# Performance work log

Measured on AMD Instinct MI355X. Metric: run time of the kernel, lower is better.

Reference implementation:

```python
import jax, jax.numpy as jnp
import numpy as np
from jax import lax

# Config mirrors TemporalLePEAttention(dim=256, resolution=(56,56), idx=0, split_size=4, num_heads=8, temporal=True)
B, T, H, W, C = 2, 2, 56, 56, 256
NH = 8
HD = C // NH
SS = 4                      # split_size
H_sp, W_sp = H, SS          # idx == 0 -> strip windows of full height
nWh, nWw = H // H_sp, W // W_sp   # 1, 14
SCALE = HD ** -0.5
KH, KW = W_sp, H_sp         # unfold kernel = focal_window = [W_sp, H_sp] = (4, 56)
PH, PW = 0, H_sp // 2       # idx == 0 padding = [0, H_sp//2]
NW = B * nWh * nWw          # number of windows
TQ = T * H_sp * W_sp        # query tokens per window


def setup_inputs() -> dict:
    key = jax.random.key(0)
    k1, k2 = jax.random.split(key, 2)
    qkv = jax.random.normal(k1, (3, B, T, H, W, C), jnp.float32)
    # depthwise 3x3 LePE conv (nn.Conv2d(dim, dim, 3, padding=1, groups=dim))
    get_v_w = jax.random.normal(k2, (C, 1, 3, 3), jnp.float32) * 0.1
    get_v_b = jnp.zeros((C,), jnp.float32)
    # pool linear initialized as in the module: weight = SS/(H_sp*W_sp), bias = 0
    pool_w = jnp.full((SS, H_sp * W_sp), SS / (H_sp * W_sp), jnp.float32)
    pool_b = jnp.zeros((SS,), jnp.float32)
    return {"qkv": qkv, "get_v_w": get_v_w, "get_v_b": get_v_b,
            "pool_w": pool_w, "pool_b": pool_b}


def _windows_thw(x):
    # im2ddca_temporal: (B,T,H,W,C) -> (B*nWh*nWw, NH, T*H_sp*W_sp, HD)
    x = x.reshape(B, T, nWh, H_sp, nWw, W_sp, C).transpose(0, 2, 4, 1, 3, 5, 6)
    x = x.reshape(NW, TQ, NH, HD).transpose(0, 2, 1, 3)
    return x


def _lepe_temporal(v, w, b):
    # get_lepe_temporal: window v, depthwise 3x3 conv, return (v_win, lepe) as (NW, NH, TQ, HD)
    xw = v.reshape(B, T, nWh, H_sp, nWw, W_sp, C).transpose(0, 2, 4, 1, 6, 3, 5)
    xw = xw.reshape(-1, C, H_sp, W_sp)  # (B*nWh*nWw*T, C, H_sp, W_sp)
    lepe = lax.conv_general_dilated(xw, w, (1, 1), 'SAME', feature_group_count=C,
                                    dimension_numbers=('NCHW', 'OIHW', 'NCHW'))
    lepe = lepe + b[None, :, None, None]

    def fmt(t):
        t = t.reshape(NW, T, NH, HD, H_sp * W_sp).transpose(0, 2, 1, 4, 3)
        return t.reshape(NW, NH, TQ, HD)
    return fmt(xw), fmt(lepe)


def _pool_unfold(t, pool_w, pool_b):
    # focal pooling: per-window linear over H_sp*W_sp -> SS, then unfold over pooled map
    tw = t.reshape(B, T, nWh, H_sp, nWw, W_sp, C).transpose(0, 2, 4, 1, 6, 3, 5)
    tw = tw.reshape(B, nWh, nWw, T, C, H_sp * W_sp)
    p = jnp.einsum('bhwtcn,sn->bhwtcs', tw, pool_w) + pool_b  # (B,nWh,nWw,T,C,SS)
    # flatten(-2) + permute + reshape -> pooled map (B*T, C, SS*nWh, nWw)  (idx == 0)
    pm = p.transpose(0, 3, 4, 5, 1, 2).reshape(B * T, C, SS * nWh, nWw)
    # nn.Unfold(kernel=(KH,KW), padding=(PH,PW), stride=1); here out_h == 1
    pmp = jnp.pad(pm, ((0, 0), (0, 0), (PH, PH), (PW, PW)))
    ow = pmp.shape[3] - KW + 1  # = nWw + 1
    patches = jnp.stack([pmp[:, :, :, i:i + KW] for i in range(ow)], axis=1)  # (BT, ow, C, KH, KW)
    u = patches.reshape(B, T, ow, C, KH, KW).transpose(0, 2, 1, 4, 5, 3)      # (B, ow, T, KH, KW, C)
    u = u.reshape(B * ow, T * KH * KW, NH, HD).transpose(0, 2, 1, 3)          # (B*ow, NH, Tkk, HD)
    # idx == 0: view (B, nWh, -1, ...) and drop the last unfold location -> one per window
    u = u.reshape(B, nWh, ow // nWh, NH, T * KH * KW, HD)[:, :, :-1]
    return u.reshape(NW, NH, T * KH * KW, HD)


def reference(qkv, get_v_w, get_v_b, pool_w, pool_b):
    q_in, k_in, v_in = qkv[0], qkv[1], qkv[2]
    q = _windows_thw(q_in) * SCALE                      # (NW, NH, TQ, HD)
    k = _windows_thw(k_in)
    v, lepe = _lepe_temporal(v_in, get_v_w, get_v_b)
    kp = _pool_unfold(k_in, pool_w, pool_b)             # (NW, NH, TQ, HD)
    vp = _pool_unfold(v_in, pool_w, pool_b)
    k = jnp.concatenate([k, kp], axis=2)                # (NW, NH, 2*TQ, HD)
    v = jnp.concatenate([v, vp], axis=2)
    attn = jax.nn.softmax(jnp.einsum('wnqd,wnkd->wnqk', q, k), axis=-1)
    x = jnp.einsum('wnqk,wnkd->wnqd', attn, v) + lepe   # (NW, NH, TQ, HD)
    x = x.transpose(0, 2, 1, 3).reshape(NW, TQ, C)
    # windows2img_temporal -> (B, T, H, W, C)
    x = x.reshape(B, nWh, nWw, T, H_sp, W_sp, C).transpose(0, 3, 1, 4, 2, 5, 6)
    return x.reshape(B, T, H, W, C)
```

## Files before the change

kernel.cpp:

```cpp
#include <hip/hip_runtime.h>
#include <hip/hip_bf16.h>

#define B_    2
#define T_    2
#define H_    56
#define W_    56
#define C_    256
#define NWW_  14
#define WC_   (W_ * C_)
#define P1_   (H_ * W_ * C_)
#define NWIN_ 448
#define NPOOL_ 128
#define VIRT_ 320.0f
#define MEXP_ 16.0f

typedef __bf16 bf16;
typedef __bf16 bf16x8 __attribute__((ext_vector_type(8)));
typedef __bf16 bf16x4 __attribute__((ext_vector_type(4)));
typedef float  f32x4  __attribute__((ext_vector_type(4)));
typedef short  s16x4  __attribute__((ext_vector_type(4)));
typedef short  s16x8  __attribute__((ext_vector_type(8)));
typedef unsigned int  uint;
typedef uint   uint4v __attribute__((ext_vector_type(4)));
typedef uint   uint2v __attribute__((ext_vector_type(2)));
typedef unsigned short u16;

__device__ __forceinline__ uint pack2(float a, float b) {
    u16 ha = __builtin_bit_cast(u16, (bf16)a);
    u16 hb = __builtin_bit_cast(u16, (bf16)b);
    return (uint)ha | ((uint)hb << 16);
}
__device__ __forceinline__ s16x4 pack4(float a, float b, float c, float d) {
    const uint2v u = {pack2(a, b), pack2(c, d)};
    return __builtin_bit_cast(s16x4, u);
}

__launch_bounds__(1024, 1)
__global__ void pre_kernel(const float* __restrict__ k_in, const float* __restrict__ v_in,
                           const float* __restrict__ pool_w, const float* __restrict__ pool_b,
                           const float* __restrict__ gw, const float* __restrict__ gb,
                           bf16* __restrict__ kw, bf16* __restrict__ vw,
                           bf16* __restrict__ lepew, bf16* __restrict__ kp,
                           bf16* __restrict__ vp) {
    __shared__ float pws[4][224];
    __shared__ float red[3][4][2][256];
    __shared__ u16  tileT[256 * 33];

    const int bid = blockIdx.x;
    const int tid = threadIdx.x;

    if (bid < 56) {
        const int j = bid % NWW_;
        const int t = (bid / NWW_) % T_;
        const int b = bid / (NWW_ * T_);
        const int quarter = tid >> 8;
        const int c = tid & 255;
        const int nh = c >> 5, hd = c & 31;
        const int bn = b * 8 + nh;

        if (tid < 896) pws[tid / 224][tid % 224] = pool_w[tid];
        __syncthreads();

        float ak[4] = {0.f, 0.f, 0.f, 0.f};
        float av[4] = {0.f, 0.f, 0.f, 0.f};
        const int n0 = quarter * 56;
        #pragma unroll 4
        for (int i = 0; i < 56; ++i) {
            const int n = n0 + i;
            const int h = n >> 2, wi = n & 3;
            const size_t off = (size_t)(b * T_ + t) * P1_ + h * WC_ + (j * 4 + wi) * C_ + c;
            const float kv = k_in[off];
            const float vv = v_in[off];
            #pragma unroll
            for (int s = 0; s < 4; ++s) {
                ak[s] += kv * pws[s][n];
                av[s] += vv * pws[s][n];
            }
        }
        if (quarter > 0) {
            #pragma unroll
            for (int s = 0; s < 4; ++s) {
                red[quarter - 1][s][0][c] = ak[s];
                red[quarter - 1][s][1][c] = av[s];
            }
        }
        __syncthreads();
        if (quarter == 0) {
            #pragma unroll
            for (int s = 0; s < 4; ++s) {
                const float bias = pool_b[s];
                const float sk = ak[s] + red[0][s][0][c] + red[1][s][0][c] + red[2][s][0][c] + bias;
                const float sv = av[s] + red[0][s][1][c] + red[1][s][1][c] + red[2][s][1][c] + bias;
                const int n = t * 56 + s * 14 + j;
                kp[((size_t)bn * NPOOL_ + n) * 32 + hd] = (bf16)sk;
                const int i5 = n & 31;
                const int slot = ((i5 & 15) >> 2) * 8 + (i5 >> 4) * 4 + (i5 & 3);
                vp[(((size_t)bn * 4 + (n >> 5)) * 32 + hd) * 32 + slot] = (bf16)sv;
            }
        }
        if (t == 0 && j == 0) {
            for (int z = tid; z < 2048; z += 1024) {
                const int nh2 = z >> 8, off = z & 255;
                ((uint*)kp)[((size_t)(b * 8 + nh2) * NPOOL_ + 112) * 16 + off] = 0u;
            }
            {
                const int z = tid;
                const int nh2 = z >> 7, hd2 = (z >> 2) & 31, gg = z & 3;
                const size_t base16 = (((size_t)(b * 8 + nh2) * 4 + 3) * 32 + hd2) * 32 + gg * 8 + 4;
                ((uint*)vp)[base16 / 2]     = 0u;
                ((uint*)vp)[base16 / 2 + 1] = 0u;
            }
        }
    } else {
        const int r  = bid - 56;
        const int rc = r % 7;
        const int ww = (r / 7) % NWW_;
        const int t  = (r / 98) % T_;
        const int b  = r / 196;
        const int hs = tid >> 8;
        const int c  = tid & 255;
        const int nh = c >> 5, hd = c & 31;
        const size_t bt = (size_t)(b * T_ + t) * P1_;
        const size_t winbase = ((size_t)((b * 8 + nh) * NWW_ + ww)) * NWIN_ * 32;

        float wv9[9];
        #pragma unroll
        for (int k = 0; k < 9; ++k) wv9[k] = gw[c * 9 + k];
        const float bias = gb[c];

        float tile[4][4];
        #pragma unroll
        for (int dy = 0; dy < 4; ++dy) {
            const int hh = rc * 8 + hs * 2 - 1 + dy;
            const bool ok = (hh >= 0 && hh < H_);
            #pragma unroll
            for (int x = 0; x < 4; ++x)
                tile[dy][x] = ok ? v_in[bt + hh * WC_ + (ww * 4 + x) * C_ + c] : 0.f;
        }

        #pragma unroll
        for (int e = 0; e < 2; ++e) {
            const int h = rc * 8 + hs * 2 + e;
            #pragma unroll
            for (int wi = 0; wi < 4; ++wi) {
                const int tokc = hs * 8 + e * 4 + wi;
                const int tokw = t * 224 + h * 4 + wi;
                float acc = bias;
                #pragma unroll
                for (int dy = 0; dy < 3; ++dy) {
                    #pragma unroll
                    for (int dx = -1; dx <= 1; ++dx) {
                        const int xx = wi + dx;
                        if (xx >= 0 && xx < 4)
                            acc += wv9[dy * 3 + dx + 1] * tile[e + dy][xx];
                    }
                }
                lepew[winbase + (size_t)tokw * 32 + hd] = (bf16)acc;
                kw[winbase + (size_t)tokw * 32 + hd] =
                    (bf16)k_in[bt + h * WC_ + (ww * 4 + wi) * C_ + c];
                tileT[c * 33 + tokc] = __builtin_bit_cast(u16, (bf16)tile[1 + e][wi]);
            }
        }
        __syncthreads();

        const int ch = t * 7 + rc;
        #pragma unroll
        for (int rep = 0; rep < 4; ++rep) {
            const int u  = tid + rep * 1024;
            const int cc = u >> 4;
            const int p  = u & 15;
            const int tok0 = ((p >> 1) & 1) * 16 + (p >> 2) * 4 + ((2 * p) & 3);
            const uint val = (uint)tileT[cc * 33 + tok0] |
                             ((uint)tileT[cc * 33 + tok0 + 1] << 16);
            const size_t dst = (((size_t)((b * 8 + (cc >> 5)) * NWW_ + ww)) * 14 + ch) * 1024
                             + (cc & 31) * 32;
            ((uint*)vw)[dst / 2 + p] = val;
        }
    }
}

__launch_bounds__(256, 6)
__global__ void attn_kernel(const float* __restrict__ q_in, const bf16* __restrict__ kw,
                            const bf16* __restrict__ vw, const bf16* __restrict__ lepew,
                            const bf16* __restrict__ kp, const bf16* __restrict__ vp,
                            float* __restrict__ out) {
    const int tid  = threadIdx.x;
    const int lane = tid & 63;
    const int phys = blockIdx.x;
    const int xcd  = phys & 7;
    const int slot = phys >> 3;
    const int hw   = xcd * 28 + slot / 7;
    const int qt   = (slot % 7) * 4 + (tid >> 6);
    const int nh   = hw & 7;
    const int nwi  = hw >> 3;
    const int b    = nwi / NWW_;
    const int ww   = nwi % NWW_;
    const int l15  = lane & 15;
    const int g    = lane >> 4;
    const int bn   = b * 8 + nh;
    const int cbase = nh * 32;
    const float QS = 0.17677669529663687f * 1.4426950408889634f;

    bf16x8 qf;
    {
        const int qrow = qt * 16 + l15;
        const int t = qrow / 224, r = qrow % 224;
        const int h = r >> 2, wi = r & 3;
        const size_t off = (size_t)(b * T_ + t) * P1_ + h * WC_ + (ww * 4 + wi) * C_ + cbase + g * 8;
        const f32x4 a0 = *(const f32x4*)(q_in + off);
        const f32x4 a1 = *(const f32x4*)(q_in + off + 4);
        const uint4v qp = {pack2(a0[0] * QS, a0[1] * QS), pack2(a0[2] * QS, a0[3] * QS),
                           pack2(a1[0] * QS, a1[1] * QS), pack2(a1[2] * QS, a1[3] * QS)};
        qf = __builtin_bit_cast(bf16x8, qp);
    }

    f32x4 o0 = {0.f, 0.f, 0.f, 0.f}, o1 = {0.f, 0.f, 0.f, 0.f};
    float ssum = 0.f;
    const f32x4 zf = {0.f, 0.f, 0.f, 0.f};

    auto computeFull = [&](const bf16x8& KA, const bf16x8& KB,
                           const bf16x8& VA, const bf16x8& VB) {
        const f32x4 s0 = __builtin_amdgcn_mfma_f32_16x16x32_bf16(KA, qf, zf, 0, 0, 0);
        const f32x4 s1 = __builtin_amdgcn_mfma_f32_16x16x32_bf16(KB, qf, zf, 0, 0, 0);
        const float p0 = __builtin_amdgcn_exp2f(s0[0] - MEXP_);
        const float p1 = __builtin_amdgcn_exp2f(s0[1] - MEXP_);
        const float p2 = __builtin_amdgcn_exp2f(s0[2] - MEXP_);
        const float p3 = __builtin_amdgcn_exp2f(s0[3] - MEXP_);
        const float p4 = __builtin_amdgcn_exp2f(s1[0] - MEXP_);
        const float p5 = __builtin_amdgcn_exp2f(s1[1] - MEXP_);
        const float p6 = __builtin_amdgcn_exp2f(s1[2] - MEXP_);
        const float p7 = __builtin_amdgcn_exp2f(s1[3] - MEXP_);
        ssum += ((p0 + p1) + (p2 + p3)) + ((p4 + p5) + (p6 + p7));
        const s16x4 pb0 = pack4(p0, p1, p2, p3);
        const s16x4 pb1 = pack4(p4, p5, p6, p7);
        const s16x8 va = __builtin_bit_cast(s16x8, VA);
        const s16x8 vb = __builtin_bit_cast(s16x8, VB);
        const s16x4 v00 = {va[0], va[1], va[2], va[3]};
        const s16x4 v01 = {va[4], va[5], va[6], va[7]};
        const s16x4 v10 = {vb[0], vb[1], vb[2], vb[3]};
        const s16x4 v11 = {vb[4], vb[5], vb[6], vb[7]};
        o0 = __builtin_amdgcn_mfma_f32_16x16x16bf16_1k(v00, pb0, o0, 0, 0, 0);
        o0 = __builtin_amdgcn_mfma_f32_16x16x16bf16_1k(v01, pb1, o0, 0, 0, 0);
        o1 = __builtin_amdgcn_mfma_f32_16x16x16bf16_1k(v10, pb0, o1, 0, 0, 0);
        o1 = __builtin_amdgcn_mfma_f32_16x16x16bf16_1k(v11, pb1, o1, 0, 0, 0);
    };

    const bf16* kwb = kw + ((size_t)(bn * NWW_ + ww)) * NWIN_ * 32;
    const bf16* vwb = vw + ((size_t)(bn * NWW_ + ww)) * 14 * 1024;
    const int ko = l15 * 32 + g * 8;
    const int ko2 = (16 + l15) * 32 + g * 8;
    #pragma unroll 2
    for (int ch = 0; ch < 14; ++ch) {
        const bf16x8 ka = *(const bf16x8*)(kwb + ch * 1024 + ko);
        const bf16x8 kb = *(const bf16x8*)(kwb + ch * 1024 + ko2);
        const bf16x8 vA = *(const bf16x8*)(vwb + ch * 1024 + ko);
        const bf16x8 vB = *(const bf16x8*)(vwb + ch * 1024 + ko2);
        computeFull(ka, kb, vA, vB);
    }

    const bf16* kpb = kp + (size_t)bn * NPOOL_ * 32;
    const bf16* vpb = vp + (size_t)bn * 4 * 1024;
    #pragma unroll 2
    for (int pc = 0; pc < 4; ++pc) {
        const bf16x8 ka = *(const bf16x8*)(kpb + pc * 1024 + ko);
        const bf16x8 kb = *(const bf16x8*)(kpb + pc * 1024 + ko2);
        const bf16x8 vA = *(const bf16x8*)(vpb + pc * 1024 + ko);
        const bf16x8 vB = *(const bf16x8*)(vpb + pc * 1024 + ko2);
        computeFull(ka, kb, vA, vB);
    }

    float den = ssum;
    den += __shfl_xor(den, 16);
    den += __shfl_xor(den, 32);
    den += VIRT_ * 0.0000152587890625f;
    const float osc = 1.0f / den;

    const int qrow = qt * 16 + l15;
    const bf16* lw = lepew + ((size_t)(bn * NWW_ + ww)) * NWIN_ * 32 + (size_t)qrow * 32;
    const bf16x4 lp0 = *(const bf16x4*)(lw + g * 4);
    const bf16x4 lp1 = *(const bf16x4*)(lw + 16 + g * 4);

    const int t = qrow / 224, rr = qrow % 224;
    const int h = rr >> 2, wi = rr & 3;
    const size_t off = (size_t)(b * T_ + t) * P1_ + h * WC_ + (ww * 4 + wi) * C_ + cbase;
    f32x4 val0, val1;
    #pragma unroll
    for (int r = 0; r < 4; ++r) {
        val0[r] = o0[r] * osc + (float)lp0[r];
        val1[r] = o1[r] * osc + (float)lp1[r];
    }
    *(f32x4*)(out + off + g * 4)      = val0;
    *(f32x4*)(out + off + 16 + g * 4) = val1;
}

extern "C" void kernel_launch(void* const* d_in, const int* in_sizes, int n_in,
                              void* d_out, int out_size, void* d_ws, size_t ws_size,
                              hipStream_t stream) {
    const float* qkv = (const float*)d_in[0];
    const float* gw  = (const float*)d_in[1];
    const float* gb  = (const float*)d_in[2];
    const float* pw  = (const float*)d_in[3];
    const float* pb  = (const float*)d_in[4];

    const size_t plane = (size_t)B_ * T_ * H_ * W_ * C_;
    const float* q_in = qkv;
    const float* k_in = qkv + plane;
    const float* v_in = qkv + 2 * plane;

    bf16* kw    = (bf16*)d_ws;
    bf16* vw    = kw + plane;
    bf16* lepew = vw + plane;
    bf16* kp    = lepew + plane;
    bf16* vp    = kp + (size_t)16 * NPOOL_ * 32;
    float* outp = (float*)d_out;

    hipLaunchKernelGGL(pre_kernel, dim3(56 + 392), dim3(1024), 0, stream,
                       k_in, v_in, pw, pb, gw, gb, kw, vw, lepew, kp, vp);
    hipLaunchKernelGGL(attn_kernel, dim3(1568), dim3(256), 0, stream,
                       q_in, kw, vw, lepew, kp, vp, outp);
}
```

Measured before the change: 52.76 us.

## Fuse pooling into conv pre-pass, store LePE to output, two query tiles per wave

The separate pooling blocks are removed. Pooled K/V partial sums are now accumulated inside the conv/window pre-pass blocks, which run with 256 threads, and a small finalize kernel reduces the seven partials. LePE is written as fp32 straight into the output buffer and read back in the attention epilogue, replacing the bf16 LePE workspace. The attention kernel now processes two query tiles per wave, so each K/V load is reused twice, with 448-thread blocks and fewer blocks overall. This adds a third kernel launch, more registers per thread in attention and lower block-level parallelism.

```diff
diff --git a/kernel.cpp b/kernel.cpp
--- a/kernel.cpp
+++ b/kernel.cpp
@@ -11,12 +11,12 @@
 #define P1_   (H_ * W_ * C_)
 #define NWIN_ 448
 #define NPOOL_ 128
+#define PMSZ_ 57344
 #define VIRT_ 320.0f
 #define MEXP_ 16.0f
 
 typedef __bf16 bf16;
 typedef __bf16 bf16x8 __attribute__((ext_vector_type(8)));
-typedef __bf16 bf16x4 __attribute__((ext_vector_type(4)));
 typedef float  f32x4  __attribute__((ext_vector_type(4)));
 typedef short  s16x4  __attribute__((ext_vector_type(4)));
 typedef short  s16x8  __attribute__((ext_vector_type(8)));
@@ -35,99 +35,39 @@
     return __builtin_bit_cast(s16x4, u);
 }
 
-__launch_bounds__(1024, 1)
+__launch_bounds__(256, 4)
 __global__ void pre_kernel(const float* __restrict__ k_in, const float* __restrict__ v_in,
-                           const float* __restrict__ pool_w, const float* __restrict__ pool_b,
+                           const float* __restrict__ pool_w,
                            const float* __restrict__ gw, const float* __restrict__ gb,
                            bf16* __restrict__ kw, bf16* __restrict__ vw,
-                           bf16* __restrict__ lepew, bf16* __restrict__ kp,
-                           bf16* __restrict__ vp) {
+                           float* __restrict__ lep_out,
+                           float* __restrict__ pmk_part, float* __restrict__ pmv_part) {
     __shared__ float pws[4][224];
-    __shared__ float red[3][4][2][256];
     __shared__ u16  tileT[256 * 33];
 
     const int bid = blockIdx.x;
     const int tid = threadIdx.x;
-
-    if (bid < 56) {
-        const int j = bid % NWW_;
-        const int t = (bid / NWW_) % T_;
-        const int b = bid / (NWW_ * T_);
-        const int quarter = tid >> 8;
-        const int c = tid & 255;
-        const int nh = c >> 5, hd = c & 31;
-        const int bn = b * 8 + nh;
-
-        if (tid < 896) pws[tid / 224][tid % 224] = pool_w[tid];
-        __syncthreads();
-
-        float ak[4] = {0.f, 0.f, 0.f, 0.f};
-        float av[4] = {0.f, 0.f, 0.f, 0.f};
-        const int n0 = quarter * 56;
-        #pragma unroll 4
-        for (int i = 0; i < 56; ++i) {
-            const int n = n0 + i;
-            const int h = n >> 2, wi = n & 3;
-            const size_t off = (size_t)(b * T_ + t) * P1_ + h * WC_ + (j * 4 + wi) * C_ + c;
-            const float kv = k_in[off];
-            const float vv = v_in[off];
-            #pragma unroll
-            for (int s = 0; s < 4; ++s) {
-                ak[s] += kv * pws[s][n];
-                av[s] += vv * pws[s][n];
-            }
-        }
-        if (quarter > 0) {
-            #pragma unroll
-            for (int s = 0; s < 4; ++s) {
-                red[quarter - 1][s][0][c] = ak[s];
-                red[quarter - 1][s][1][c] = av[s];
-            }
-        }
-        __syncthreads();
-        if (quarter == 0) {
-            #pragma unroll
-            for (int s = 0; s < 4; ++s) {
-                const float bias = pool_b[s];
-                const float sk = ak[s] + red[0][s][0][c] + red[1][s][0][c] + red[2][s][0][c] + bias;
-                const float sv = av[s] + red[0][s][1][c] + red[1][s][1][c] + red[2][s][1][c] + bias;
-                const int n = t * 56 + s * 14 + j;
-                kp[((size_t)bn * NPOOL_ + n) * 32 + hd] = (bf16)sk;
-                const int i5 = n & 31;
-                const int slot = ((i5 & 15) >> 2) * 8 + (i5 >> 4) * 4 + (i5 & 3);
-                vp[(((size_t)bn * 4 + (n >> 5)) * 32 + hd) * 32 + slot] = (bf16)sv;
-            }
-        }
-        if (t == 0 && j == 0) {
-            for (int z = tid; z < 2048; z += 1024) {
-                const int nh2 = z >> 8, off = z & 255;
-                ((uint*)kp)[((size_t)(b * 8 + nh2) * NPOOL_ + 112) * 16 + off] = 0u;
-            }
-            {
-                const int z = tid;
-                const int nh2 = z >> 7, hd2 = (z >> 2) & 31, gg = z & 3;
-                const size_t base16 = (((size_t)(b * 8 + nh2) * 4 + 3) * 32 + hd2) * 32 + gg * 8 + 4;
-                ((uint*)vp)[base16 / 2]     = 0u;
-                ((uint*)vp)[base16 / 2 + 1] = 0u;
-            }
-        }
-    } else {
-        const int r  = bid - 56;
-        const int rc = r % 7;
-        const int ww = (r / 7) % NWW_;
-        const int t  = (r / 98) % T_;
-        const int b  = r / 196;
-        const int hs = tid >> 8;
-        const int c  = tid & 255;
-        const int nh = c >> 5, hd = c & 31;
-        const size_t bt = (size_t)(b * T_ + t) * P1_;
-        const size_t winbase = ((size_t)((b * 8 + nh) * NWW_ + ww)) * NWIN_ * 32;
-
-        float wv9[9];
-        #pragma unroll
-        for (int k = 0; k < 9; ++k) wv9[k] = gw[c * 9 + k];
-        const float bias = gb[c];
-
+    const int rc = bid % 7;
+    const int ww = (bid / 7) % NWW_;
+    const int t  = (bid / 98) % T_;
+    const int b  = bid / 196;
+    const int c  = tid;
+    const int nh = c >> 5, hd = c & 31;
+    const size_t bt = (size_t)(b * T_ + t) * P1_;
+    const size_t winbase = ((size_t)((b * 8 + nh) * NWW_ + ww)) * NWIN_ * 32;
+
+    for (int i = tid; i < 896; i += 256) pws[i / 224][i % 224] = pool_w[i];
+    __syncthreads();
+
+    float wv9[9];
+    #pragma unroll
+    for (int k = 0; k < 9; ++k) wv9[k] = gw[c * 9 + k];
+    const float bias = gb[c];
+
+    float pk[4] = {0.f, 0.f, 0.f, 0.f};
+    float pv[4] = {0.f, 0.f, 0.f, 0.f};
+
+    for (int hs = 0; hs < 4; ++hs) {
         float tile[4][4];
         #pragma unroll
         for (int dy = 0; dy < 4; ++dy) {
@@ -137,7 +77,6 @@
             for (int x = 0; x < 4; ++x)
                 tile[dy][x] = ok ? v_in[bt + hh * WC_ + (ww * 4 + x) * C_ + c] : 0.f;
         }
-
         #pragma unroll
         for (int e = 0; e < 2; ++e) {
             const int h = rc * 8 + hs * 2 + e;
@@ -155,42 +94,91 @@
                             acc += wv9[dy * 3 + dx + 1] * tile[e + dy][xx];
                     }
                 }
-                lepew[winbase + (size_t)tokw * 32 + hd] = (bf16)acc;
-                kw[winbase + (size_t)tokw * 32 + hd] =
-                    (bf16)k_in[bt + h * WC_ + (ww * 4 + wi) * C_ + c];
-                tileT[c * 33 + tokc] = __builtin_bit_cast(u16, (bf16)tile[1 + e][wi]);
+                lep_out[bt + h * WC_ + (ww * 4 + wi) * C_ + c] = acc;
+                const float kv = k_in[bt + h * WC_ + (ww * 4 + wi) * C_ + c];
+                kw[winbase + (size_t)tokw * 32 + hd] = (bf16)kv;
+                const float vv = tile[1 + e][wi];
+                const int n = h * 4 + wi;
+                #pragma unroll
+                for (int s = 0; s < 4; ++s) {
+                    pk[s] += kv * pws[s][n];
+                    pv[s] += vv * pws[s][n];
+                }
+                tileT[c * 33 + tokc] = __builtin_bit_cast(u16, (bf16)vv);
             }
         }
-        __syncthreads();
-
-        const int ch = t * 7 + rc;
-        #pragma unroll
-        for (int rep = 0; rep < 4; ++rep) {
-            const int u  = tid + rep * 1024;
-            const int cc = u >> 4;
-            const int p  = u & 15;
-            const int tok0 = ((p >> 1) & 1) * 16 + (p >> 2) * 4 + ((2 * p) & 3);
-            const uint val = (uint)tileT[cc * 33 + tok0] |
-                             ((uint)tileT[cc * 33 + tok0 + 1] << 16);
-            const size_t dst = (((size_t)((b * 8 + (cc >> 5)) * NWW_ + ww)) * 14 + ch) * 1024
-                             + (cc & 31) * 32;
-            ((uint*)vw)[dst / 2 + p] = val;
-        }
-    }
-}
-
-__launch_bounds__(256, 6)
+    }
+
+    #pragma unroll
+    for (int s = 0; s < 4; ++s) {
+        const size_t o = (size_t)rc * PMSZ_ +
+                         ((size_t)(((b * T_ + t) * 4 + s) * NWW_ + ww)) * C_ + c;
+        pmk_part[o] = pk[s];
+        pmv_part[o] = pv[s];
+    }
+
+    __syncthreads();
+
+    const int ch = t * 7 + rc;
+    #pragma unroll
+    for (int rep = 0; rep < 16; ++rep) {
+        const int u  = tid + rep * 256;
+        const int cc = u >> 4;
+        const int p  = u & 15;
+        const int tok0 = ((p >> 1) & 1) * 16 + (p >> 2) * 4 + ((2 * p) & 3);
+        const uint val = (uint)tileT[cc * 33 + tok0] |
+                         ((uint)tileT[cc * 33 + tok0 + 1] << 16);
+        const size_t dst = (((size_t)((b * 8 + (cc >> 5)) * NWW_ + ww)) * 14 + ch) * 1024
+                         + (cc & 31) * 32;
+        ((uint*)vw)[dst / 2 + p] = val;
+    }
+}
+
+__global__ void finalize_kernel(const float* __restrict__ pmk_part,
+                                const float* __restrict__ pmv_part,
+                                const float* __restrict__ pool_b,
+                                bf16* __restrict__ kp, bf16* __restrict__ vp) {
+    const int bn = blockIdx.x;
+    const int b  = bn >> 3, nh = bn & 7;
+    const int tid = threadIdx.x;
+    const int hd = tid & 31;
+    const int c  = nh * 32 + hd;
+
+    for (int n = tid >> 5; n < 112; n += 8) {
+        const int t = n / 56, r = n % 56;
+        const int s = r / 14, j = r % 14;
+        const size_t base = ((size_t)(((b * T_ + t) * 4 + s) * NWW_ + j)) * C_ + c;
+        float sk = pool_b[s], sv = pool_b[s];
+        #pragma unroll
+        for (int rc = 0; rc < 7; ++rc) {
+            sk += pmk_part[(size_t)rc * PMSZ_ + base];
+            sv += pmv_part[(size_t)rc * PMSZ_ + base];
+        }
+        kp[((size_t)bn * NPOOL_ + n) * 32 + hd] = (bf16)sk;
+        const int i5 = n & 31;
+        const int slot = ((i5 & 15) >> 2) * 8 + (i5 >> 4) * 4 + (i5 & 3);
+        vp[(((size_t)bn * 4 + (n >> 5)) * 32 + hd) * 32 + slot] = (bf16)sv;
+    }
+    for (int z = tid; z < 512; z += 256)
+        kp[((size_t)bn * NPOOL_ + 112) * 32 + z] = (bf16)0.f;
+    for (int z = tid; z < 512; z += 256) {
+        const int hd2 = z >> 4, idx = z & 15;
+        vp[(((size_t)bn * 4 + 3) * 32 + hd2) * 32 + ((idx >> 2) * 8 + 4 + (idx & 3))] = (bf16)0.f;
+    }
+}
+
+__launch_bounds__(448, 4)
 __global__ void attn_kernel(const float* __restrict__ q_in, const bf16* __restrict__ kw,
-                            const bf16* __restrict__ vw, const bf16* __restrict__ lepew,
-                            const bf16* __restrict__ kp, const bf16* __restrict__ vp,
-                            float* __restrict__ out) {
+                            const bf16* __restrict__ vw, const bf16* __restrict__ kp,
+                            const bf16* __restrict__ vp, float* __restrict__ out) {
     const int tid  = threadIdx.x;
     const int lane = tid & 63;
+    const int wv   = tid >> 6;
     const int phys = blockIdx.x;
     const int xcd  = phys & 7;
-    const int slot = phys >> 3;
-    const int hw   = xcd * 28 + slot / 7;
-    const int qt   = (slot % 7) * 4 + (tid >> 6);
+    const int sl   = phys >> 3;
+    const int hw   = xcd * 28 + (sl >> 1);
+    const int half = sl & 1;
     const int nh   = hw & 7;
     const int nwi  = hw >> 3;
     const int b    = nwi / NWW_;
@@ -199,11 +187,13 @@
     const int g    = lane >> 4;
     const int bn   = b * 8 + nh;
     const int cbase = nh * 32;
+    const int tbase = half * 14 + wv;
     const float QS = 0.17677669529663687f * 1.4426950408889634f;
 
-    bf16x8 qf;
-    {
-        const int qrow = qt * 16 + l15;
+    bf16x8 qf[2];
+    #pragma unroll
+    for (int ti = 0; ti < 2; ++ti) {
+        const int qrow = (tbase + ti * 7) * 16 + l15;
         const int t = qrow / 224, r = qrow % 224;
         const int h = r >> 2, wi = r & 3;
         const size_t off = (size_t)(b * T_ + t) * P1_ + h * WC_ + (ww * 4 + wi) * C_ + cbase + g * 8;
@@ -211,86 +201,81 @@
         const f32x4 a1 = *(const f32x4*)(q_in + off + 4);
         const uint4v qp = {pack2(a0[0] * QS, a0[1] * QS), pack2(a0[2] * QS, a0[3] * QS),
                            pack2(a1[0] * QS, a1[1] * QS), pack2(a1[2] * QS, a1[3] * QS)};
-        qf = __builtin_bit_cast(bf16x8, qp);
-    }
-
-    f32x4 o0 = {0.f, 0.f, 0.f, 0.f}, o1 = {0.f, 0.f, 0.f, 0.f};
-    float ssum = 0.f;
+        qf[ti] = __builtin_bit_cast(bf16x8, qp);
+    }
+
+    f32x4 o[2][2];
+    float ssum[2];
     const f32x4 zf = {0.f, 0.f, 0.f, 0.f};
-
-    auto computeFull = [&](const bf16x8& KA, const bf16x8& KB,
-                           const bf16x8& VA, const bf16x8& VB) {
-        const f32x4 s0 = __builtin_amdgcn_mfma_f32_16x16x32_bf16(KA, qf, zf, 0, 0, 0);
-        const f32x4 s1 = __builtin_amdgcn_mfma_f32_16x16x32_bf16(KB, qf, zf, 0, 0, 0);
-        const float p0 = __builtin_amdgcn_exp2f(s0[0] - MEXP_);
-        const float p1 = __builtin_amdgcn_exp2f(s0[1] - MEXP_);
-        const float p2 = __builtin_amdgcn_exp2f(s0[2] - MEXP_);
-        const float p3 = __builtin_amdgcn_exp2f(s0[3] - MEXP_);
-        const float p4 = __builtin_amdgcn_exp2f(s1[0] - MEXP_);
-        const float p5 = __builtin_amdgcn_exp2f(s1[1] - MEXP_);
-        const float p6 = __builtin_amdgcn_exp2f(s1[2] - MEXP_);
-        const float p7 = __builtin_amdgcn_exp2f(s1[3] - MEXP_);
-        ssum += ((p0 + p1) + (p2 + p3)) + ((p4 + p5) + (p6 + p7));
-        const s16x4 pb0 = pack4(p0, p1, p2, p3);
-        const s16x4 pb1 = pack4(p4, p5, p6, p7);
-        const s16x8 va = __builtin_bit_cast(s16x8, VA);
-        const s16x8 vb = __builtin_bit_cast(s16x8, VB);
+    #pragma unroll
+    for (int ti = 0; ti < 2; ++ti) { o[ti][0] = zf; o[ti][1] = zf; ssum[ti] = 0.f; }
+
+    const bf16* kwb = kw + ((size_t)(bn * NWW_ + ww)) * NWIN_ * 32;
+    const bf16* vwb = vw + ((size_t)(bn * NWW_ + ww)) * 14 * 1024;
+    const bf16* kpb = kp + (size_t)bn * NPOOL_ * 32;
+    const bf16* vpb = vp + (size_t)bn * 4 * 1024;
+    const int ko  = l15 * 32 + g * 8;
+    const int ko2 = (16 + l15) * 32 + g * 8;
+
+    auto compute = [&](const bf16* kc, const bf16* vc) {
+        const bf16x8 ka = *(const bf16x8*)(kc + ko);
+        const bf16x8 kb = *(const bf16x8*)(kc + ko2);
+        const s16x8 va = __builtin_bit_cast(s16x8, *(const bf16x8*)(vc + ko));
+        const s16x8 vb = __builtin_bit_cast(s16x8, *(const bf16x8*)(vc + ko2));
         const s16x4 v00 = {va[0], va[1], va[2], va[3]};
         const s16x4 v01 = {va[4], va[5], va[6], va[7]};
         const s16x4 v10 = {vb[0], vb[1], vb[2], vb[3]};
         const s16x4 v11 = {vb[4], vb[5], vb[6], vb[7]};
-        o0 = __builtin_amdgcn_mfma_f32_16x16x16bf16_1k(v00, pb0, o0, 0, 0, 0);
-        o0 = __builtin_amdgcn_mfma_f32_16x16x16bf16_1k(v01, pb1, o0, 0, 0, 0);
-        o1 = __builtin_amdgcn_mfma_f32_16x16x16bf16_1k(v10, pb0, o1, 0, 0, 0);
-        o1 = __builtin_amdgcn_mfma_f32_16x16x16bf16_1k(v11, pb1, o1, 0, 0, 0);
+        #pragma unroll
+        for (int ti = 0; ti < 2; ++ti) {
+            const f32x4 s0 = __builtin_amdgcn_mfma_f32_16x16x32_bf16(ka, qf[ti], zf, 0, 0, 0);
+            const f32x4 s1 = __builtin_amdgcn_mfma_f32_16x16x32_bf16(kb, qf[ti], zf, 0, 0, 0);
+            const float p0 = __builtin_amdgcn_exp2f(s0[0] - MEXP_);
+            const float p1 = __builtin_amdgcn_exp2f(s0[1] - MEXP_);
+            const float p2 = __builtin_amdgcn_exp2f(s0[2] - MEXP_);
+            const float p3 = __builtin_amdgcn_exp2f(s0[3] - MEXP_);
+            const float p4 = __builtin_amdgcn_exp2f(s1[0] - MEXP_);
+            const float p5 = __builtin_amdgcn_exp2f(s1[1] - MEXP_);
+            const float p6 = __builtin_amdgcn_exp2f(s1[2] - MEXP_);
+            const float p7 = __builtin_amdgcn_exp2f(s1[3] - MEXP_);
+            ssum[ti] += ((p0 + p1) + (p2 + p3)) + ((p4 + p5) + (p6 + p7));
+            const s16x4 pb0 = pack4(p0, p1, p2, p3);
+            const s16x4 pb1 = pack4(p4, p5, p6, p7);
+            o[ti][0] = __builtin_amdgcn_mfma_f32_16x16x16bf16_1k(v00, pb0, o[ti][0], 0, 0, 0);
+            o[ti][0] = __builtin_amdgcn_mfma_f32_16x16x16bf16_1k(v01, pb1, o[ti][0], 0, 0, 0);
+            o[ti][1] = __builtin_amdgcn_mfma_f32_16x16x16bf16_1k(v10, pb0, o[ti][1], 0, 0, 0);
+            o[ti][1] = __builtin_amdgcn_mfma_f32_16x16x16bf16_1k(v11, pb1, o[ti][1], 0, 0, 0);
+        }
     };
 
-    const bf16* kwb = kw + ((size_t)(bn * NWW_ + ww)) * NWIN_ * 32;
-    const bf16* vwb = vw + ((size_t)(bn * NWW_ + ww)) * 14 * 1024;
-    const int ko = l15 * 32 + g * 8;
-    const int ko2 = (16 + l15) * 32 + g * 8;
-    #pragma unroll 2
-    for (int ch = 0; ch < 14; ++ch) {
-        const bf16x8 ka = *(const bf16x8*)(kwb + ch * 1024 + ko);
-        const bf16x8 kb = *(const bf16x8*)(kwb + ch * 1024 + ko2);
-        const bf16x8 vA = *(const bf16x8*)(vwb + ch * 1024 + ko);
-        const bf16x8 vB = *(const bf16x8*)(vwb + ch * 1024 + ko2);
-        computeFull(ka, kb, vA, vB);
-    }
-
-    const bf16* kpb = kp + (size_t)bn * NPOOL_ * 32;
-    const bf16* vpb = vp + (size_t)bn * 4 * 1024;
-    #pragma unroll 2
-    for (int pc = 0; pc < 4; ++pc) {
-        const bf16x8 ka = *(const bf16x8*)(kpb + pc * 1024 + ko);
-        const bf16x8 kb = *(const bf16x8*)(kpb + pc * 1024 + ko2);
-        const bf16x8 vA = *(const bf16x8*)(vpb + pc * 1024 + ko);
-        const bf16x8 vB = *(const bf16x8*)(vpb + pc * 1024 + ko2);
-        computeFull(ka, kb, vA, vB);
-    }
-
-    float den = ssum;
-    den += __shfl_xor(den, 16);
-    den += __shfl_xor(den, 32);
-    den += VIRT_ * 0.0000152587890625f;
-    const float osc = 1.0f / den;
-
-    const int qrow = qt * 16 + l15;
-    const bf16* lw = lepew + ((size_t)(bn * NWW_ + ww)) * NWIN_ * 32 + (size_t)qrow * 32;
-    const bf16x4 lp0 = *(const bf16x4*)(lw + g * 4);
-    const bf16x4 lp1 = *(const bf16x4*)(lw + 16 + g * 4);
-
-    const int t = qrow / 224, rr = qrow % 224;
-    const int h = rr >> 2, wi = rr & 3;
-    const size_t off = (size_t)(b * T_ + t) * P1_ + h * WC_ + (ww * 4 + wi) * C_ + cbase;
-    f32x4 val0, val1;
-    #pragma unroll
-    for (int r = 0; r < 4; ++r) {
-        val0[r] = o0[r] * osc + (float)lp0[r];
-        val1[r] = o1[r] * osc + (float)lp1[r];
-    }
-    *(f32x4*)(out + off + g * 4)      = val0;
-    *(f32x4*)(out + off + 16 + g * 4) = val1;
+    #pragma unroll
+    for (int ch = 0; ch < 14; ++ch) compute(kwb + ch * 1024, vwb + ch * 1024);
+    #pragma unroll
+    for (int pc = 0; pc < 4; ++pc)  compute(kpb + pc * 1024, vpb + pc * 1024);
+
+    #pragma unroll
+    for (int ti = 0; ti < 2; ++ti) {
+        float den = ssum[ti];
+        den += __shfl_xor(den, 16);
+        den += __shfl_xor(den, 32);
+        den += VIRT_ * 0.0000152587890625f;
+        const float osc = 1.0f / den;
+
+        const int qrow = (tbase + ti * 7) * 16 + l15;
+        const int t = qrow / 224, rr = qrow % 224;
+        const int h = rr >> 2, wi = rr & 3;
+        const size_t off = (size_t)(b * T_ + t) * P1_ + h * WC_ + (ww * 4 + wi) * C_ + cbase;
+        const f32x4 lp0 = *(const f32x4*)(out + off + g * 4);
+        const f32x4 lp1 = *(const f32x4*)(out + off + 16 + g * 4);
+        f32x4 val0, val1;
+        #pragma unroll
+        for (int r = 0; r < 4; ++r) {
+            val0[r] = o[ti][0][r] * osc + lp0[r];
+            val1[r] = o[ti][1][r] * osc + lp1[r];
+        }
+        *(f32x4*)(out + off + g * 4)      = val0;
+        *(f32x4*)(out + off + 16 + g * 4) = val1;
+    }
 }
 
 extern "C" void kernel_launch(void* const* d_in, const int* in_sizes, int n_in,
@@ -307,15 +292,18 @@
     const float* k_in = qkv + plane;
     const float* v_in = qkv + 2 * plane;
 
-    bf16* kw    = (bf16*)d_ws;
-    bf16* vw    = kw + plane;
-    bf16* lepew = vw + plane;
-    bf16* kp    = lepew + plane;
-    bf16* vp    = kp + (size_t)16 * NPOOL_ * 32;
+    bf16* kw = (bf16*)d_ws;
+    bf16* vw = kw + plane;
+    bf16* kp = vw + plane;
+    bf16* vp = kp + (size_t)16 * NPOOL_ * 32;
+    float* pmk_part = (float*)(vp + (size_t)16 * NPOOL_ * 32);
+    float* pmv_part = pmk_part + 7 * (size_t)PMSZ_;
     float* outp = (float*)d_out;
 
-    hipLaunchKernelGGL(pre_kernel, dim3(56 + 392), dim3(1024), 0, stream,
-                       k_in, v_in, pw, pb, gw, gb, kw, vw, lepew, kp, vp);
-    hipLaunchKernelGGL(attn_kernel, dim3(1568), dim3(256), 0, stream,
-                       q_in, kw, vw, lepew, kp, vp, outp);
-}
+    hipLaunchKernelGGL(pre_kernel, dim3(392), dim3(256), 0, stream,
+                       k_in, v_in, pw, gw, gb, kw, vw, outp, pmk_part, pmv_part);
+    hipLaunchKernelGGL(finalize_kernel, dim3(16), dim3(256), 0, stream,
+                       pmk_part, pmv_part, pb, kp, vp);
+    hipLaunchKernelGGL(attn_kernel, dim3(448), dim3(448), 0, stream,
+                       q_in, kw, vw, kp, vp, outp);
+}
```

After: 62.73 us. +18.9%, slower.
